# Performance work log

Measured on AMD Instinct MI355X. Metric: run time of the kernel, lower is better.

## Reference

```python
import jax, jax.numpy as jnp
import numpy as np
from jax import lax

B, T, D = 4096, 2048, 8
NUM_LAYERS = 6  # hidden_size = 1


def setup_inputs() -> dict:
    key = jax.random.key(0)
    ks = jax.random.split(key, 6)
    u = lambda k, shape: jax.random.uniform(k, shape, jnp.float32, -1.0, 1.0)  # pytorch init: U(-1/sqrt(H), 1/sqrt(H)), H=1
    return {
        "x": jax.random.normal(ks[0], (B, T, D), jnp.float32),
        "W_ih0": u(ks[1], (3, D)),            # layer 0 input weights [3*H, D], H=1
        "W_ih_rest": u(ks[2], (NUM_LAYERS - 1, 3)),  # layers 1..5 input weights [3*H, 1] squeezed
        "W_hh": u(ks[3], (NUM_LAYERS, 3)),    # hidden weights [3*H, H] squeezed (H=1)
        "b_ih": u(ks[4], (NUM_LAYERS, 3)),
        "b_hh": u(ks[5], (NUM_LAYERS, 3)),
    }


def _gru_layer(xp, w_hh, b_hh):
    # xp: [B, T, 3] precomputed input-gate projections (W_ih @ x + b_ih)
    # w_hh, b_hh: [3] scalar hidden weights/biases (hidden_size == 1)
    def step(h, xp_t):  # h: [B], xp_t: [B, 3]
        r = jax.nn.sigmoid(xp_t[:, 0] + w_hh[0] * h + b_hh[0])
        z = jax.nn.sigmoid(xp_t[:, 1] + w_hh[1] * h + b_hh[1])
        n = jnp.tanh(xp_t[:, 2] + r * (w_hh[2] * h + b_hh[2]))
        h_new = (1.0 - z) * n + z * h
        return h_new, h_new

    h0 = jnp.zeros(xp.shape[0], xp.dtype)
    _, ys = lax.scan(step, h0, jnp.swapaxes(xp, 0, 1))  # ys: [T, B]
    return jnp.swapaxes(ys, 0, 1)  # [B, T]


def reference(x, W_ih0, W_ih_rest, W_hh, b_ih, b_hh):
    # Layer 0: project D-dim input to the 3 gates once, then scan over time.
    xp = jnp.einsum('btd,gd->btg', x, W_ih0) + b_ih[0]  # [B, T, 3]
    h_seq = _gru_layer(xp, W_hh[0], b_hh[0])            # [B, T]
    # Layers 1..5: scalar input (previous layer's hidden), hidden_size=1.
    # Dropout(0.5) between layers is inference-mode identity here.
    for l in range(1, NUM_LAYERS):
        xp = h_seq[:, :, None] * W_ih_rest[l - 1][None, None, :] + b_ih[l]  # [B, T, 3]
        h_seq = _gru_layer(xp, W_hh[l], b_hh[l])
    # y[:, -1, 0] -> last timestep of last layer
    return h_seq[:, -1]
```

## Files before the change

kernel.cpp:

```cpp
#include <hip/hip_runtime.h>


#define T_LEN 2048
#define T8    (T_LEN * 8)
#define NCH   256

typedef __attribute__((ext_vector_type(2))) float v2f;

__device__ __forceinline__ float dpp_shr1(float v) {
    int i = __builtin_bit_cast(int, v);
    int r = __builtin_amdgcn_update_dpp(0, i, 0x111, 0xF, 0xF, true);
    return __builtin_bit_cast(float, r);
}
__device__ __forceinline__ float dpp_shl1(float v) {
    int i = __builtin_bit_cast(int, v);
    int r = __builtin_amdgcn_update_dpp(0, i, 0x101, 0xF, 0xF, true);
    return __builtin_bit_cast(float, r);
}

__global__ __launch_bounds__(64)
__attribute__((amdgpu_waves_per_eu(1, 1)))
void gru_scan(const float* __restrict__ x,
              const float* __restrict__ Wih0,
              const float* __restrict__ Wrest,
              const float* __restrict__ Whh,
              const float* __restrict__ bih,
              const float* __restrict__ bhh,
              float* __restrict__ out)
{
    const int lane = threadIdx.x & 63;
    const int l    = lane & 7;
    const int g    = lane >> 3;
    const int b    = blockIdx.x * 8 + g;

    const float c1 = -1.44269504088896340736f;
    const float cz =  1.44269504088896340736f;
    const float c2 = 2.0f * c1;

    const int  lidx = l < 6 ? l : 5;
    const bool lz   = (l == 0);
    const float m1  = lz ? 0.0f : 1.0f;

    const float whpr = c1 * Whh[lidx * 3 + 0];
    const float whpz = cz * Whh[lidx * 3 + 1];
    const float whpn = c2 * Whh[lidx * 3 + 2];
    const float bhpn = c2 * bhh[lidx * 3 + 2];
    const v2f  WH12 = {whpr, whpz};

    const int ir = lidx >= 1 ? lidx - 1 : 0;
    const float W1r = m1 * c1 * Wrest[ir * 3 + 0];
    const float W1z = m1 * cz * Wrest[ir * 3 + 1];
    const float W1n = m1 * c2 * Wrest[ir * 3 + 2];
    const v2f  W1rz = {W1r, W1z};
    const float B1r = c1 * (bih[lidx * 3 + 0] + bhh[lidx * 3 + 0]);
    const float B1z = cz * (bih[lidx * 3 + 1] + bhh[lidx * 3 + 1]);
    const float B1n = c2 *  bih[lidx * 3 + 2];
    const v2f  B1rz = {B1r, B1z};

    const v2f  B0rz = {c1 * (bih[0] + bhh[0]), cz * (bih[1] + bhh[1])};
    const float B0n = c2 * bih[2];
    v2f  wrz[8];
    float wn[8];
    #pragma unroll
    for (int d = 0; d < 8; ++d) {
        wrz[d] = (v2f){c1 * Wih0[d], cz * Wih0[8 + d]};
        wn[d]  = c2 * Wih0[16 + d];
    }

    const float4* xp = reinterpret_cast<const float4*>(x + (size_t)b * T8) + (lane & 7) * 2;

    float4 L0a, L0b, L1a, L1b, L2a, L2b, L3a, L3b;
    v2f   PRZ;
    float PN;
    float belt_r, belt_z, belt_n;
    float h = 0.0f;

#define LOADL(A, B, C)                                                        \
    { const int cc_ = ((C) < NCH) ? (C) : 0;                                  \
      const float4* p_ = xp + (size_t)cc_ * 16;                               \
      A = p_[0]; B = p_[1]; }

#define GETF(S, A, B) ((S)==0?(A).x:(S)==1?(A).y:(S)==2?(A).z:(S)==3?(A).w:  \
                       (S)==4?(B).x:(S)==5?(B).y:(S)==6?(B).z:(B).w)

#define DOT_SLICE(S, LA, LB)                                                  \
    { const float xv_ = GETF(S, LA, LB);                                      \
      if ((S) == 0) { PRZ = wrz[0] * (v2f){xv_, xv_} + B0rz;                  \
                      PN  = fmaf(xv_, wn[0], B0n); }                          \
      else          { PRZ = wrz[S] * (v2f){xv_, xv_} + PRZ;                   \
                      PN  = fmaf(xv_, wn[S], PN); } }

    auto step1 = [&](int i, v2f brz, float bn, bool guard) {
        const float nbr = dpp_shr1(h);

        const v2f t12 = WH12 * (v2f){h, h} + brz;
        const v2f arz = W1rz * (v2f){nbr, nbr} + t12;
        const float er = __builtin_amdgcn_exp2f(arz.x);
        const float ez = __builtin_amdgcn_exp2f(arz.y);
        const float r  = __builtin_amdgcn_rcpf(1.0f + er);
        const float pz1 = 1.0f + ez;

        const v2f tnx = (v2f){whpn, W1n} * (v2f){h, nbr} + (v2f){bhpn, bn};
        const float na = fmaf(r, tnx.x, tnx.y);
        const float en = __builtin_amdgcn_exp2f(na);
        const float pn1 = 1.0f + en;

        const float P  = pn1 * pz1;
        const float R  = __builtin_amdgcn_rcpf(P);
        const float hp1 = h + 1.0f;
        const float hm1 = 1.0f - h;
        const float q  = fmaf(-hp1, en, hm1);
        const float hn = fmaf(R, q, h);

        if (guard) {
            h = ((unsigned)(i - l) < (unsigned)T_LEN) ? hn : h;
        } else {
            h = hn;
        }
    };

#define STEP_B(S, C, LNa, LNb, GD)                                            \
    { const v2f  brz_ = lz ? (v2f){belt_r, belt_z} : B1rz;                    \
      const float bn_ = lz ? belt_n : B1n;                                    \
      step1((C) * 8 + (S), brz_, bn_, GD);                                    \
      DOT_SLICE(S, LNa, LNb)                                                  \
      belt_r = dpp_shl1(belt_r);                                              \
      belt_z = dpp_shl1(belt_z);                                              \
      belt_n = dpp_shl1(belt_n); }

#define RUN_CHUNK(C, LNa, LNb, LlA, LlB, C4, GD)                              \
    { LOADL(LlA, LlB, C4)                                                     \
      STEP_B(0, C, LNa, LNb, GD) STEP_B(1, C, LNa, LNb, GD)                   \
      STEP_B(2, C, LNa, LNb, GD) STEP_B(3, C, LNa, LNb, GD)                   \
      STEP_B(4, C, LNa, LNb, GD) STEP_B(5, C, LNa, LNb, GD)                   \
      STEP_B(6, C, LNa, LNb, GD) STEP_B(7, C, LNa, LNb, GD)                   \
      belt_r = PRZ.x; belt_z = PRZ.y; belt_n = PN; }

    LOADL(L0a, L0b, 0) LOADL(L1a, L1b, 1) LOADL(L2a, L2b, 2)

    DOT_SLICE(0, L0a, L0b) DOT_SLICE(1, L0a, L0b)
    DOT_SLICE(2, L0a, L0b) DOT_SLICE(3, L0a, L0b)
    DOT_SLICE(4, L0a, L0b) DOT_SLICE(5, L0a, L0b)
    DOT_SLICE(6, L0a, L0b) DOT_SLICE(7, L0a, L0b)
    belt_r = PRZ.x; belt_z = PRZ.y; belt_n = PN;

    RUN_CHUNK(0, L1a, L1b, L3a, L3b, 3, true)
    RUN_CHUNK(1, L2a, L2b, L0a, L0b, 4, false)
    RUN_CHUNK(2, L3a, L3b, L1a, L1b, 5, false)
    RUN_CHUNK(3, L0a, L0b, L2a, L2b, 6, false)

    #pragma unroll 1
    for (int q = 1; q < 64; ++q) {
        const int c0 = q * 4;
        RUN_CHUNK(c0 + 0, L1a, L1b, L3a, L3b, c0 + 3, false)
        RUN_CHUNK(c0 + 1, L2a, L2b, L0a, L0b, c0 + 4, false)
        RUN_CHUNK(c0 + 2, L3a, L3b, L1a, L1b, c0 + 5, false)
        RUN_CHUNK(c0 + 3, L0a, L0b, L2a, L2b, c0 + 6, false)
    }

    #pragma unroll
    for (int i = T_LEN; i < T_LEN + 5; ++i) step1(i, B1rz, B1n, true);

    if (l == 5) out[b] = h;
}

extern "C" void kernel_launch(void* const* d_in, const int* in_sizes, int n_in,
                              void* d_out, int out_size, void* d_ws, size_t ws_size,
                              hipStream_t stream) {
    const float* x     = (const float*)d_in[0];
    const float* Wih0  = (const float*)d_in[1];
    const float* Wrest = (const float*)d_in[2];
    const float* Whh   = (const float*)d_in[3];
    const float* bih   = (const float*)d_in[4];
    const float* bhh   = (const float*)d_in[5];
    float* out = (float*)d_out;

    gru_scan<<<512, 64, 0, stream>>>(x, Wih0, Wrest, Whh, bih, bhh, out);
}
```

Baseline: 152.3 us.

## Precompute per-step layer-0 gate biases one chunk ahead via direct DPP shifts

Replaces the serial belt of three DPP left-shifts per step with per-step preselected bias arrays computed one chunk ahead, using DPP row shifts by S directly from the finished projection. The projection pipeline is deepened by one chunk with double-buffered accumulators, and the load prefetch distance grows to four chunks. The aim is to take the belt shifts and select operations off the recurrence's critical path. The step also fuses (1+en)*pz1 into a single fma. The cost is more live registers (16 v2f plus 16 floats of staged biases) and a longer prologue.

```diff
diff --git a/kernel.cpp b/kernel.cpp
--- a/kernel.cpp
+++ b/kernel.cpp
@@ -12,11 +12,11 @@
     int r = __builtin_amdgcn_update_dpp(0, i, 0x111, 0xF, 0xF, true);
     return __builtin_bit_cast(float, r);
 }
-__device__ __forceinline__ float dpp_shl1(float v) {
-    int i = __builtin_bit_cast(int, v);
-    int r = __builtin_amdgcn_update_dpp(0, i, 0x101, 0xF, 0xF, true);
-    return __builtin_bit_cast(float, r);
-}
+
+#define DPPSHL(S, v) __builtin_bit_cast(float,                                \
+    __builtin_amdgcn_update_dpp(0, __builtin_bit_cast(int, (v)),              \
+                                0x100 | ((S) == 0 ? 1 : (S)), 0xF, 0xF, true))
+#define DPPSHLX(S, v) ((S) == 0 ? (v) : DPPSHL(S, v))
 
 __global__ __launch_bounds__(64)
 __attribute__((amdgpu_waves_per_eu(1, 1)))
@@ -70,9 +70,10 @@
     const float4* xp = reinterpret_cast<const float4*>(x + (size_t)b * T8) + (lane & 7) * 2;
 
     float4 L0a, L0b, L1a, L1b, L2a, L2b, L3a, L3b;
-    v2f   PRZ;
-    float PN;
-    float belt_r, belt_z, belt_n;
+    v2f   PZArz, PZBrz;
+    float PZAn,  PZBn;
+    v2f   SrzA[8], SrzB[8];
+    float SnA[8],  SnB[8];
     float h = 0.0f;
 
 #define LOADL(A, B, C)                                                        \
@@ -83,12 +84,19 @@
 #define GETF(S, A, B) ((S)==0?(A).x:(S)==1?(A).y:(S)==2?(A).z:(S)==3?(A).w:  \
                        (S)==4?(B).x:(S)==5?(B).y:(S)==6?(B).z:(B).w)
 
-#define DOT_SLICE(S, LA, LB)                                                  \
+#define DOT_SLICE(S, LA, LB, PRZ, PN)                                         \
     { const float xv_ = GETF(S, LA, LB);                                      \
       if ((S) == 0) { PRZ = wrz[0] * (v2f){xv_, xv_} + B0rz;                  \
                       PN  = fmaf(xv_, wn[0], B0n); }                          \
       else          { PRZ = wrz[S] * (v2f){xv_, xv_} + PRZ;                   \
                       PN  = fmaf(xv_, wn[S], PN); } }
+
+#define PRESEL(S, SRZ, SN, PRZs, PNs)                                         \
+    { const float br_ = DPPSHLX(S, (PRZs).x);                                 \
+      const float bz_ = DPPSHLX(S, (PRZs).y);                                 \
+      const float bn_ = DPPSHLX(S, (PNs));                                    \
+      SRZ[S] = (v2f){lz ? br_ : B1r, lz ? bz_ : B1z};                         \
+      SN[S]  = lz ? bn_ : B1n; }
 
     auto step1 = [&](int i, v2f brz, float bn, bool guard) {
         const float nbr = dpp_shr1(h);
@@ -103,9 +111,8 @@
         const v2f tnx = (v2f){whpn, W1n} * (v2f){h, nbr} + (v2f){bhpn, bn};
         const float na = fmaf(r, tnx.x, tnx.y);
         const float en = __builtin_amdgcn_exp2f(na);
-        const float pn1 = 1.0f + en;
 
-        const float P  = pn1 * pz1;
+        const float P  = fmaf(en, pz1, pz1);
         const float R  = __builtin_amdgcn_rcpf(P);
         const float hp1 = h + 1.0f;
         const float hm1 = 1.0f - h;
@@ -119,43 +126,53 @@
         }
     };
 
-#define STEP_B(S, C, LNa, LNb, GD)                                            \
-    { const v2f  brz_ = lz ? (v2f){belt_r, belt_z} : B1rz;                    \
-      const float bn_ = lz ? belt_n : B1n;                                    \
-      step1((C) * 8 + (S), brz_, bn_, GD);                                    \
-      DOT_SLICE(S, LNa, LNb)                                                  \
-      belt_r = dpp_shl1(belt_r);                                              \
-      belt_z = dpp_shl1(belt_z);                                              \
-      belt_n = dpp_shl1(belt_n); }
+#define STEPX(S, C, SRr, SNr, SRw, SNw, PZr_rz, PZr_n, PZw_rz, PZw_n,         \
+              LNa, LNb, GD)                                                   \
+    { step1((C) * 8 + (S), SRr[S], SNr[S], GD);                               \
+      DOT_SLICE(S, LNa, LNb, PZw_rz, PZw_n)                                   \
+      PRESEL(S, SRw, SNw, PZr_rz, PZr_n) }
 
-#define RUN_CHUNK(C, LNa, LNb, LlA, LlB, C4, GD)                              \
+#define RUN_CHUNK(C, SRr, SNr, SRw, SNw, PZr_rz, PZr_n, PZw_rz, PZw_n,        \
+                  LNa, LNb, LlA, LlB, C4, GD)                                 \
     { LOADL(LlA, LlB, C4)                                                     \
-      STEP_B(0, C, LNa, LNb, GD) STEP_B(1, C, LNa, LNb, GD)                   \
-      STEP_B(2, C, LNa, LNb, GD) STEP_B(3, C, LNa, LNb, GD)                   \
-      STEP_B(4, C, LNa, LNb, GD) STEP_B(5, C, LNa, LNb, GD)                   \
-      STEP_B(6, C, LNa, LNb, GD) STEP_B(7, C, LNa, LNb, GD)                   \
-      belt_r = PRZ.x; belt_z = PRZ.y; belt_n = PN; }
+      STEPX(0, C, SRr, SNr, SRw, SNw, PZr_rz, PZr_n, PZw_rz, PZw_n, LNa, LNb, GD) \
+      STEPX(1, C, SRr, SNr, SRw, SNw, PZr_rz, PZr_n, PZw_rz, PZw_n, LNa, LNb, GD) \
+      STEPX(2, C, SRr, SNr, SRw, SNw, PZr_rz, PZr_n, PZw_rz, PZw_n, LNa, LNb, GD) \
+      STEPX(3, C, SRr, SNr, SRw, SNw, PZr_rz, PZr_n, PZw_rz, PZw_n, LNa, LNb, GD) \
+      STEPX(4, C, SRr, SNr, SRw, SNw, PZr_rz, PZr_n, PZw_rz, PZw_n, LNa, LNb, GD) \
+      STEPX(5, C, SRr, SNr, SRw, SNw, PZr_rz, PZr_n, PZw_rz, PZw_n, LNa, LNb, GD) \
+      STEPX(6, C, SRr, SNr, SRw, SNw, PZr_rz, PZr_n, PZw_rz, PZw_n, LNa, LNb, GD) \
+      STEPX(7, C, SRr, SNr, SRw, SNw, PZr_rz, PZr_n, PZw_rz, PZw_n, LNa, LNb, GD) }
 
-    LOADL(L0a, L0b, 0) LOADL(L1a, L1b, 1) LOADL(L2a, L2b, 2)
+    LOADL(L0a, L0b, 0) LOADL(L1a, L1b, 1) LOADL(L2a, L2b, 2) LOADL(L3a, L3b, 3)
 
-    DOT_SLICE(0, L0a, L0b) DOT_SLICE(1, L0a, L0b)
-    DOT_SLICE(2, L0a, L0b) DOT_SLICE(3, L0a, L0b)
-    DOT_SLICE(4, L0a, L0b) DOT_SLICE(5, L0a, L0b)
-    DOT_SLICE(6, L0a, L0b) DOT_SLICE(7, L0a, L0b)
-    belt_r = PRZ.x; belt_z = PRZ.y; belt_n = PN;
+    DOT_SLICE(0, L0a, L0b, PZArz, PZAn) DOT_SLICE(1, L0a, L0b, PZArz, PZAn)
+    DOT_SLICE(2, L0a, L0b, PZArz, PZAn) DOT_SLICE(3, L0a, L0b, PZArz, PZAn)
+    DOT_SLICE(4, L0a, L0b, PZArz, PZAn) DOT_SLICE(5, L0a, L0b, PZArz, PZAn)
+    DOT_SLICE(6, L0a, L0b, PZArz, PZAn) DOT_SLICE(7, L0a, L0b, PZArz, PZAn)
 
-    RUN_CHUNK(0, L1a, L1b, L3a, L3b, 3, true)
-    RUN_CHUNK(1, L2a, L2b, L0a, L0b, 4, false)
-    RUN_CHUNK(2, L3a, L3b, L1a, L1b, 5, false)
-    RUN_CHUNK(3, L0a, L0b, L2a, L2b, 6, false)
+    DOT_SLICE(0, L1a, L1b, PZBrz, PZBn) DOT_SLICE(1, L1a, L1b, PZBrz, PZBn)
+    DOT_SLICE(2, L1a, L1b, PZBrz, PZBn) DOT_SLICE(3, L1a, L1b, PZBrz, PZBn)
+    DOT_SLICE(4, L1a, L1b, PZBrz, PZBn) DOT_SLICE(5, L1a, L1b, PZBrz, PZBn)
+    DOT_SLICE(6, L1a, L1b, PZBrz, PZBn) DOT_SLICE(7, L1a, L1b, PZBrz, PZBn)
+
+    PRESEL(0, SrzA, SnA, PZArz, PZAn) PRESEL(1, SrzA, SnA, PZArz, PZAn)
+    PRESEL(2, SrzA, SnA, PZArz, PZAn) PRESEL(3, SrzA, SnA, PZArz, PZAn)
+    PRESEL(4, SrzA, SnA, PZArz, PZAn) PRESEL(5, SrzA, SnA, PZArz, PZAn)
+    PRESEL(6, SrzA, SnA, PZArz, PZAn) PRESEL(7, SrzA, SnA, PZArz, PZAn)
+
+    RUN_CHUNK(0, SrzA, SnA, SrzB, SnB, PZBrz, PZBn, PZArz, PZAn, L2a, L2b, L0a, L0b, 4, true)
+    RUN_CHUNK(1, SrzB, SnB, SrzA, SnA, PZArz, PZAn, PZBrz, PZBn, L3a, L3b, L1a, L1b, 5, false)
+    RUN_CHUNK(2, SrzA, SnA, SrzB, SnB, PZBrz, PZBn, PZArz, PZAn, L0a, L0b, L2a, L2b, 6, false)
+    RUN_CHUNK(3, SrzB, SnB, SrzA, SnA, PZArz, PZAn, PZBrz, PZBn, L1a, L1b, L3a, L3b, 7, false)
 
     #pragma unroll 1
     for (int q = 1; q < 64; ++q) {
         const int c0 = q * 4;
-        RUN_CHUNK(c0 + 0, L1a, L1b, L3a, L3b, c0 + 3, false)
-        RUN_CHUNK(c0 + 1, L2a, L2b, L0a, L0b, c0 + 4, false)
-        RUN_CHUNK(c0 + 2, L3a, L3b, L1a, L1b, c0 + 5, false)
-        RUN_CHUNK(c0 + 3, L0a, L0b, L2a, L2b, c0 + 6, false)
+        RUN_CHUNK(c0 + 0, SrzA, SnA, SrzB, SnB, PZBrz, PZBn, PZArz, PZAn, L2a, L2b, L0a, L0b, c0 + 4, false)
+        RUN_CHUNK(c0 + 1, SrzB, SnB, SrzA, SnA, PZArz, PZAn, PZBrz, PZBn, L3a, L3b, L1a, L1b, c0 + 5, false)
+        RUN_CHUNK(c0 + 2, SrzA, SnA, SrzB, SnB, PZBrz, PZBn, PZArz, PZAn, L0a, L0b, L2a, L2b, c0 + 6, false)
+        RUN_CHUNK(c0 + 3, SrzB, SnB, SrzA, SnA, PZArz, PZAn, PZBrz, PZBn, L1a, L1b, L3a, L3b, c0 + 7, false)
     }
 
     #pragma unroll
```

Measured after the change: 148.4 us, median of 2. 2.6% less time.

## Process two batch groups per wave with packed-float recurrence and half the blocks

Applied to the files above, without the earlier changes.

Each 64-lane wave now runs two independent sequence groups (b and b+2048) and packs their hidden states into float2 vectors, so the GRU step uses packed FMA ops to interleave two independent dependency chains and hide transcendental latency. The grid drops from 512 to 256 blocks. The layer-0 bias belt shifting is replaced by a DPP shift by the slot index applied to the chunk's projection. Chunk pipelining changes to three buffers with an unroll of six. Running fewer waves risks leaving compute units idle on a many-CU GPU, and the doubled registers may reduce scheduling freedom.

```diff
diff --git a/kernel.cpp b/kernel.cpp
--- a/kernel.cpp
+++ b/kernel.cpp
@@ -12,14 +12,13 @@
     int r = __builtin_amdgcn_update_dpp(0, i, 0x111, 0xF, 0xF, true);
     return __builtin_bit_cast(float, r);
 }
-__device__ __forceinline__ float dpp_shl1(float v) {
-    int i = __builtin_bit_cast(int, v);
-    int r = __builtin_amdgcn_update_dpp(0, i, 0x101, 0xF, 0xF, true);
-    return __builtin_bit_cast(float, r);
-}
-
-__global__ __launch_bounds__(64)
-__attribute__((amdgpu_waves_per_eu(1, 1)))
+
+#define DPPSHL(S, v) __builtin_bit_cast(float,                                \
+    __builtin_amdgcn_update_dpp(0, __builtin_bit_cast(int, (v)),              \
+                                0x100 | ((S) == 0 ? 1 : (S)), 0xF, 0xF, true))
+#define DPPSHLX(S, v) ((S) == 0 ? (v) : DPPSHL(S, v))
+
+__global__ __launch_bounds__(64, 1)
 void gru_scan(const float* __restrict__ x,
               const float* __restrict__ Wih0,
               const float* __restrict__ Wrest,
@@ -31,7 +30,8 @@
     const int lane = threadIdx.x & 63;
     const int l    = lane & 7;
     const int g    = lane >> 3;
-    const int b    = blockIdx.x * 8 + g;
+    const int bA   = blockIdx.x * 8 + g;
+    const int bB   = bA + 2048;
 
     const float c1 = -1.44269504088896340736f;
     const float cz =  1.44269504088896340736f;
@@ -45,17 +45,19 @@
     const float whpz = cz * Whh[lidx * 3 + 1];
     const float whpn = c2 * Whh[lidx * 3 + 2];
     const float bhpn = c2 * bhh[lidx * 3 + 2];
-    const v2f  WH12 = {whpr, whpz};
 
     const int ir = lidx >= 1 ? lidx - 1 : 0;
     const float W1r = m1 * c1 * Wrest[ir * 3 + 0];
     const float W1z = m1 * cz * Wrest[ir * 3 + 1];
     const float W1n = m1 * c2 * Wrest[ir * 3 + 2];
-    const v2f  W1rz = {W1r, W1z};
     const float B1r = c1 * (bih[lidx * 3 + 0] + bhh[lidx * 3 + 0]);
     const float B1z = cz * (bih[lidx * 3 + 1] + bhh[lidx * 3 + 1]);
     const float B1n = c2 *  bih[lidx * 3 + 2];
-    const v2f  B1rz = {B1r, B1z};
+
+    const v2f WHPR2 = {whpr, whpr}, WHPZ2 = {whpz, whpz};
+    const v2f WHPN2 = {whpn, whpn}, BHPN2 = {bhpn, bhpn};
+    const v2f W1R2  = {W1r, W1r},   W1Z2  = {W1z, W1z},  W1N2 = {W1n, W1n};
+    const v2f B1R2  = {B1r, B1r},   B1Z2  = {B1z, B1z},  B1N2 = {B1n, B1n};
 
     const v2f  B0rz = {c1 * (bih[0] + bhh[0]), cz * (bih[1] + bhh[1])};
     const float B0n = c2 * bih[2];
@@ -67,101 +69,153 @@
         wn[d]  = c2 * Wih0[16 + d];
     }
 
-    const float4* xp = reinterpret_cast<const float4*>(x + (size_t)b * T8) + (lane & 7) * 2;
-
-    float4 L0a, L0b, L1a, L1b, L2a, L2b, L3a, L3b;
-    v2f   PRZ;
-    float PN;
-    float belt_r, belt_z, belt_n;
-    float h = 0.0f;
-
-#define LOADL(A, B, C)                                                        \
+    const float4* xpA = reinterpret_cast<const float4*>(x + (size_t)bA * T8) + (lane & 7) * 2;
+    const float4* xpB = reinterpret_cast<const float4*>(x + (size_t)bB * T8) + (lane & 7) * 2;
+
+    float4 LA0a, LA0b, LA1a, LA1b, LA2a, LA2b;
+    float4 LB0a, LB0b, LB1a, LB1b, LB2a, LB2b;
+    v2f   PZArz0, PZArz1, PZBrz0, PZBrz1;
+    float PZAn0,  PZAn1,  PZBn0,  PZBn1;
+    v2f Sr[8], Sz[8], Sn[8];
+    v2f h = {0.0f, 0.0f};
+
+#define LOADL(P, A, B, C)                                                     \
     { const int cc_ = ((C) < NCH) ? (C) : 0;                                  \
-      const float4* p_ = xp + (size_t)cc_ * 16;                               \
+      const float4* p_ = P + (size_t)cc_ * 16;                                \
       A = p_[0]; B = p_[1]; }
 
 #define GETF(S, A, B) ((S)==0?(A).x:(S)==1?(A).y:(S)==2?(A).z:(S)==3?(A).w:  \
                        (S)==4?(B).x:(S)==5?(B).y:(S)==6?(B).z:(B).w)
 
-#define DOT_SLICE(S, LA, LB)                                                  \
+#define DOT_SLICE(S, LA, LB, PRZ, PN)                                         \
     { const float xv_ = GETF(S, LA, LB);                                      \
       if ((S) == 0) { PRZ = wrz[0] * (v2f){xv_, xv_} + B0rz;                  \
                       PN  = fmaf(xv_, wn[0], B0n); }                          \
       else          { PRZ = wrz[S] * (v2f){xv_, xv_} + PRZ;                   \
                       PN  = fmaf(xv_, wn[S], PN); } }
 
-    auto step1 = [&](int i, v2f brz, float bn, bool guard) {
-        const float nbr = dpp_shr1(h);
-
-        const v2f t12 = WH12 * (v2f){h, h} + brz;
-        const v2f arz = W1rz * (v2f){nbr, nbr} + t12;
-        const float er = __builtin_amdgcn_exp2f(arz.x);
-        const float ez = __builtin_amdgcn_exp2f(arz.y);
-        const float r  = __builtin_amdgcn_rcpf(1.0f + er);
-        const float pz1 = 1.0f + ez;
-
-        const v2f tnx = (v2f){whpn, W1n} * (v2f){h, nbr} + (v2f){bhpn, bn};
-        const float na = fmaf(r, tnx.x, tnx.y);
-        const float en = __builtin_amdgcn_exp2f(na);
-        const float pn1 = 1.0f + en;
-
-        const float P  = pn1 * pz1;
-        const float R  = __builtin_amdgcn_rcpf(P);
-        const float hp1 = h + 1.0f;
-        const float hm1 = 1.0f - h;
-        const float q  = fmaf(-hp1, en, hm1);
-        const float hn = fmaf(R, q, h);
+#define PRESELP(S, PZArz, PZAn, PZBrz, PZBn)                                  \
+    { const float brA_ = DPPSHLX(S, (PZArz).x);                               \
+      const float bzA_ = DPPSHLX(S, (PZArz).y);                               \
+      const float bnA_ = DPPSHLX(S, (PZAn));                                  \
+      const float brB_ = DPPSHLX(S, (PZBrz).x);                               \
+      const float bzB_ = DPPSHLX(S, (PZBrz).y);                               \
+      const float bnB_ = DPPSHLX(S, (PZBn));                                  \
+      Sr[S] = (v2f){lz ? brA_ : B1r, lz ? brB_ : B1r};                        \
+      Sz[S] = (v2f){lz ? bzA_ : B1z, lz ? bzB_ : B1z};                        \
+      Sn[S] = (v2f){lz ? bnA_ : B1n, lz ? bnB_ : B1n}; }
+
+    auto stepP = [&](int i, v2f br, v2f bz, v2f bn, bool guard) {
+        const v2f nbr = {dpp_shr1(h.x), dpp_shr1(h.y)};
+        const v2f one = {1.0f, 1.0f};
+
+        const v2f tr = WHPR2 * h + br;
+        const v2f ar = W1R2 * nbr + tr;
+        const v2f tz = WHPZ2 * h + bz;
+        const v2f az = W1Z2 * nbr + tz;
+
+        const v2f er = {__builtin_amdgcn_exp2f(ar.x), __builtin_amdgcn_exp2f(ar.y)};
+        const v2f ez = {__builtin_amdgcn_exp2f(az.x), __builtin_amdgcn_exp2f(az.y)};
+        const v2f pr1 = one + er;
+        const v2f r  = {__builtin_amdgcn_rcpf(pr1.x), __builtin_amdgcn_rcpf(pr1.y)};
+        const v2f pz1 = one + ez;
+
+        const v2f tn  = WHPN2 * h + BHPN2;
+        const v2f xnp = W1N2 * nbr + bn;
+        const v2f na  = r * tn + xnp;
+        const v2f en  = {__builtin_amdgcn_exp2f(na.x), __builtin_amdgcn_exp2f(na.y)};
+
+        const v2f P = en * pz1 + pz1;
+        const v2f R = {__builtin_amdgcn_rcpf(P.x), __builtin_amdgcn_rcpf(P.y)};
+
+        const v2f hp1 = h + one;
+        const v2f hm1 = one - h;
+        const v2f q   = hm1 - hp1 * en;
+        const v2f hn  = R * q + h;
 
         if (guard) {
-            h = ((unsigned)(i - l) < (unsigned)T_LEN) ? hn : h;
+            const bool ok = (unsigned)(i - l) < (unsigned)T_LEN;
+            h.x = ok ? hn.x : h.x;
+            h.y = ok ? hn.y : h.y;
         } else {
             h = hn;
         }
     };
 
-#define STEP_B(S, C, LNa, LNb, GD)                                            \
-    { const v2f  brz_ = lz ? (v2f){belt_r, belt_z} : B1rz;                    \
-      const float bn_ = lz ? belt_n : B1n;                                    \
-      step1((C) * 8 + (S), brz_, bn_, GD);                                    \
-      DOT_SLICE(S, LNa, LNb)                                                  \
-      belt_r = dpp_shl1(belt_r);                                              \
-      belt_z = dpp_shl1(belt_z);                                              \
-      belt_n = dpp_shl1(belt_n); }
-
-#define RUN_CHUNK(C, LNa, LNb, LlA, LlB, C4, GD)                              \
-    { LOADL(LlA, LlB, C4)                                                     \
-      STEP_B(0, C, LNa, LNb, GD) STEP_B(1, C, LNa, LNb, GD)                   \
-      STEP_B(2, C, LNa, LNb, GD) STEP_B(3, C, LNa, LNb, GD)                   \
-      STEP_B(4, C, LNa, LNb, GD) STEP_B(5, C, LNa, LNb, GD)                   \
-      STEP_B(6, C, LNa, LNb, GD) STEP_B(7, C, LNa, LNb, GD)                   \
-      belt_r = PRZ.x; belt_z = PRZ.y; belt_n = PN; }
-
-    LOADL(L0a, L0b, 0) LOADL(L1a, L1b, 1) LOADL(L2a, L2b, 2)
-
-    DOT_SLICE(0, L0a, L0b) DOT_SLICE(1, L0a, L0b)
-    DOT_SLICE(2, L0a, L0b) DOT_SLICE(3, L0a, L0b)
-    DOT_SLICE(4, L0a, L0b) DOT_SLICE(5, L0a, L0b)
-    DOT_SLICE(6, L0a, L0b) DOT_SLICE(7, L0a, L0b)
-    belt_r = PRZ.x; belt_z = PRZ.y; belt_n = PN;
-
-    RUN_CHUNK(0, L1a, L1b, L3a, L3b, 3, true)
-    RUN_CHUNK(1, L2a, L2b, L0a, L0b, 4, false)
-    RUN_CHUNK(2, L3a, L3b, L1a, L1b, 5, false)
-    RUN_CHUNK(3, L0a, L0b, L2a, L2b, 6, false)
+#define FSTEPP(S, C, LAra, LArb, LBra, LBrb,                                  \
+               PZWArz, PZWAn, PZWBrz, PZWBn, PZRArz, PZRAn, PZRBrz, PZRBn, GD)\
+    { stepP((C) * 8 + (S), Sr[S], Sz[S], Sn[S], GD);                          \
+      DOT_SLICE(S, LAra, LArb, PZWArz, PZWAn)                                 \
+      DOT_SLICE(S, LBra, LBrb, PZWBrz, PZWBn)                                 \
+      PRESELP(S, PZRArz, PZRAn, PZRBrz, PZRBn) }
+
+#define RUNCP(C, LAra, LArb, LBra, LBrb, LAla, LAlb, LBla, LBlb,              \
+              PZWArz, PZWAn, PZWBrz, PZWBn, PZRArz, PZRAn, PZRBrz, PZRBn, C3, GD) \
+    { LOADL(xpA, LAla, LAlb, C3) LOADL(xpB, LBla, LBlb, C3)                   \
+      FSTEPP(0, C, LAra, LArb, LBra, LBrb, PZWArz, PZWAn, PZWBrz, PZWBn, PZRArz, PZRAn, PZRBrz, PZRBn, GD) \
+      FSTEPP(1, C, LAra, LArb, LBra, LBrb, PZWArz, PZWAn, PZWBrz, PZWBn, PZRArz, PZRAn, PZRBrz, PZRBn, GD) \
+      FSTEPP(2, C, LAra, LArb, LBra, LBrb, PZWArz, PZWAn, PZWBrz, PZWBn, PZRArz, PZRAn, PZRBrz, PZRBn, GD) \
+      FSTEPP(3, C, LAra, LArb, LBra, LBrb, PZWArz, PZWAn, PZWBrz, PZWBn, PZRArz, PZRAn, PZRBrz, PZRBn, GD) \
+      FSTEPP(4, C, LAra, LArb, LBra, LBrb, PZWArz, PZWAn, PZWBrz, PZWBn, PZRArz, PZRAn, PZRBrz, PZRBn, GD) \
+      FSTEPP(5, C, LAra, LArb, LBra, LBrb, PZWArz, PZWAn, PZWBrz, PZWBn, PZRArz, PZRAn, PZRBrz, PZRBn, GD) \
+      FSTEPP(6, C, LAra, LArb, LBra, LBrb, PZWArz, PZWAn, PZWBrz, PZWBn, PZRArz, PZRAn, PZRBrz, PZRBn, GD) \
+      FSTEPP(7, C, LAra, LArb, LBra, LBrb, PZWArz, PZWAn, PZWBrz, PZWBn, PZRArz, PZRAn, PZRBrz, PZRBn, GD) }
+
+    LOADL(xpA, LA0a, LA0b, 0) LOADL(xpB, LB0a, LB0b, 0)
+    LOADL(xpA, LA1a, LA1b, 1) LOADL(xpB, LB1a, LB1b, 1)
+    LOADL(xpA, LA2a, LA2b, 2) LOADL(xpB, LB2a, LB2b, 2)
+
+#define DOT8(LA, LB, PRZ, PN)                                                 \
+    DOT_SLICE(0, LA, LB, PRZ, PN) DOT_SLICE(1, LA, LB, PRZ, PN)               \
+    DOT_SLICE(2, LA, LB, PRZ, PN) DOT_SLICE(3, LA, LB, PRZ, PN)               \
+    DOT_SLICE(4, LA, LB, PRZ, PN) DOT_SLICE(5, LA, LB, PRZ, PN)               \
+    DOT_SLICE(6, LA, LB, PRZ, PN) DOT_SLICE(7, LA, LB, PRZ, PN)
+
+    DOT8(LA0a, LA0b, PZArz0, PZAn0) DOT8(LB0a, LB0b, PZBrz0, PZBn0)
+    DOT8(LA1a, LA1b, PZArz1, PZAn1) DOT8(LB1a, LB1b, PZBrz1, PZBn1)
+
+    PRESELP(0, PZArz0, PZAn0, PZBrz0, PZBn0)
+    PRESELP(1, PZArz0, PZAn0, PZBrz0, PZBn0)
+    PRESELP(2, PZArz0, PZAn0, PZBrz0, PZBn0)
+    PRESELP(3, PZArz0, PZAn0, PZBrz0, PZBn0)
+    PRESELP(4, PZArz0, PZAn0, PZBrz0, PZBn0)
+    PRESELP(5, PZArz0, PZAn0, PZBrz0, PZBn0)
+    PRESELP(6, PZArz0, PZAn0, PZBrz0, PZBn0)
+    PRESELP(7, PZArz0, PZAn0, PZBrz0, PZBn0)
+
+    RUNCP(0, LA2a, LA2b, LB2a, LB2b, LA0a, LA0b, LB0a, LB0b,
+          PZArz0, PZAn0, PZBrz0, PZBn0, PZArz1, PZAn1, PZBrz1, PZBn1, 3, true)
+    RUNCP(1, LA0a, LA0b, LB0a, LB0b, LA1a, LA1b, LB1a, LB1b,
+          PZArz1, PZAn1, PZBrz1, PZBn1, PZArz0, PZAn0, PZBrz0, PZBn0, 4, false)
+    RUNCP(2, LA1a, LA1b, LB1a, LB1b, LA2a, LA2b, LB2a, LB2b,
+          PZArz0, PZAn0, PZBrz0, PZBn0, PZArz1, PZAn1, PZBrz1, PZBn1, 5, false)
+    RUNCP(3, LA2a, LA2b, LB2a, LB2b, LA0a, LA0b, LB0a, LB0b,
+          PZArz1, PZAn1, PZBrz1, PZBn1, PZArz0, PZAn0, PZBrz0, PZBn0, 6, false)
 
     #pragma unroll 1
-    for (int q = 1; q < 64; ++q) {
-        const int c0 = q * 4;
-        RUN_CHUNK(c0 + 0, L1a, L1b, L3a, L3b, c0 + 3, false)
-        RUN_CHUNK(c0 + 1, L2a, L2b, L0a, L0b, c0 + 4, false)
-        RUN_CHUNK(c0 + 2, L3a, L3b, L1a, L1b, c0 + 5, false)
-        RUN_CHUNK(c0 + 3, L0a, L0b, L2a, L2b, c0 + 6, false)
+    for (int qq = 0; qq < 42; ++qq) {
+        const int c0 = 4 + qq * 6;
+        RUNCP(c0 + 0, LA0a, LA0b, LB0a, LB0b, LA1a, LA1b, LB1a, LB1b,
+              PZArz0, PZAn0, PZBrz0, PZBn0, PZArz1, PZAn1, PZBrz1, PZBn1, c0 + 3, false)
+        RUNCP(c0 + 1, LA1a, LA1b, LB1a, LB1b, LA2a, LA2b, LB2a, LB2b,
+              PZArz1, PZAn1, PZBrz1, PZBn1, PZArz0, PZAn0, PZBrz0, PZBn0, c0 + 4, false)
+        RUNCP(c0 + 2, LA2a, LA2b, LB2a, LB2b, LA0a, LA0b, LB0a, LB0b,
+              PZArz0, PZAn0, PZBrz0, PZBn0, PZArz1, PZAn1, PZBrz1, PZBn1, c0 + 5, false)
+        RUNCP(c0 + 3, LA0a, LA0b, LB0a, LB0b, LA1a, LA1b, LB1a, LB1b,
+              PZArz1, PZAn1, PZBrz1, PZBn1, PZArz0, PZAn0, PZBrz0, PZBn0, c0 + 6, false)
+        RUNCP(c0 + 4, LA1a, LA1b, LB1a, LB1b, LA2a, LA2b, LB2a, LB2b,
+              PZArz0, PZAn0, PZBrz0, PZBn0, PZArz1, PZAn1, PZBrz1, PZBn1, c0 + 7, false)
+        RUNCP(c0 + 5, LA2a, LA2b, LB2a, LB2b, LA0a, LA0b, LB0a, LB0b,
+              PZArz1, PZAn1, PZBrz1, PZBn1, PZArz0, PZAn0, PZBrz0, PZBn0, c0 + 8, false)
     }
 
     #pragma unroll
-    for (int i = T_LEN; i < T_LEN + 5; ++i) step1(i, B1rz, B1n, true);
-
-    if (l == 5) out[b] = h;
+    for (int i = T_LEN; i < T_LEN + 5; ++i) stepP(i, B1R2, B1Z2, B1N2, true);
+
+    if (l == 5) {
+        out[bA] = h.x;
+        out[bB] = h.y;
+    }
 }
 
 extern "C" void kernel_launch(void* const* d_in, const int* in_sizes, int n_in,
@@ -175,5 +229,5 @@
     const float* bhh   = (const float*)d_in[5];
     float* out = (float*)d_out;
 
-    gru_scan<<<512, 64, 0, stream>>>(x, Wih0, Wrest, Whh, bih, bhh, out);
+    gru_scan<<<256, 64, 0, stream>>>(x, Wih0, Wrest, Whh, bih, bhh, out);
 }
```

Result: slower. 262.1 us (+72.1%).
